# Kernel tuning notes

Hardware: AMD Instinct MI355X
Metric: run time of the kernel (lower is better)

## Reference

```python
import jax, jax.numpy as jnp
import numpy as np

T, B, N_IN, N_OUT = 100, 32, 1024, 512
LR_LTP, LR_LTD = 1e-4, -1e-4
TAU_PRE, TAU_POST, DT = 20.0, 20.0, 1.0
W_MIN, W_MAX = 0.0, 1.0
SPIKE_PROB = 0.05


def setup_inputs() -> dict:
    key = jax.random.key(0)
    k1, k2, k3 = jax.random.split(key, 3)
    weight = jax.random.uniform(k1, (N_OUT, N_IN), dtype=jnp.float32)
    pre_spikes = (jax.random.uniform(k2, (T, B, N_IN)) < SPIKE_PROB).astype(jnp.float32)
    post_spikes = (jax.random.uniform(k3, (T, B, N_OUT)) < SPIKE_PROB).astype(jnp.float32)
    pre_trace = jnp.zeros((B, N_IN), jnp.float32)
    post_trace = jnp.zeros((B, N_OUT), jnp.float32)
    return {"weight": weight, "pre_spikes": pre_spikes, "post_spikes": post_spikes,
            "pre_trace": pre_trace, "post_trace": post_trace}


def reference(weight, pre_spikes, post_spikes, pre_trace, post_trace):
    # weight: [N_out, N_in]; pre_spikes: [T,B,N_in]; post_spikes: [T,B,N_out]
    decay_pre = jnp.exp(jnp.asarray(-DT / TAU_PRE, weight.dtype))
    decay_post = jnp.exp(jnp.asarray(-DT / TAU_POST, weight.dtype))
    # Soft bounds (w_max=1.0 > 0 -> w_max - w; w_min=0.0 not < 0 -> w)
    soft_ltp = W_MAX - weight
    soft_ltd = weight
    Bf = jnp.asarray(pre_spikes.shape[1], weight.dtype)

    def step(carry, xs):
        pre_tr, post_tr, dw = carry
        pre_s, post_s = xs  # [B,N_in], [B,N_out]
        pre_tr = pre_tr * decay_pre + pre_s
        post_tr = post_tr * decay_post + post_s
        # batch-mean of outer products -> [N_out, N_in]
        ltp_mean = jnp.einsum('bo,bi->oi', post_s, pre_tr) / Bf
        ltd_mean = jnp.einsum('bo,bi->oi', post_tr, pre_s) / Bf
        dw = dw + LR_LTP * soft_ltp * ltp_mean + LR_LTD * soft_ltd * ltd_mean
        return (pre_tr, post_tr, dw), None

    init = (pre_trace, post_trace, jnp.zeros_like(weight))
    (pre_tr, post_tr, delta_w), _ = jax.lax.scan(step, init, (pre_spikes, post_spikes))
    return delta_w, pre_tr, post_tr
```

## Files before the change

### kernel.cpp

```cpp
#include <hip/hip_runtime.h>

typedef unsigned short ushort;
typedef __attribute__((ext_vector_type(8))) short short8;
typedef __attribute__((ext_vector_type(8))) ushort ushort8;
typedef __attribute__((ext_vector_type(4))) float floatx4;

#define T_STEPS 100
#define BATCH   32
#define NIN     1024
#define NOUT    512
#define KTOT    (T_STEPS * BATCH)
#define KBYTES  (KTOT * 2)

#define LR_LTP  (1e-4f)
#define LR_LTD  (-1e-4f)
#define INV_B   (1.0f / 32.0f)
#define DECAY   0.951229424500714f

#define OFF_PRE  (NOUT * NIN)
#define OFF_POST (OFF_PRE + BATCH * NIN)

#define U_WSPRE   0
#define U_WSPOST  (U_WSPRE + KTOT * NIN)
#define U_PRST    (U_WSPOST + KTOT * NOUT)
#define U_POST_ST (U_PRST + NIN * KTOT)
#define U_PRTT    (U_POST_ST + NOUT * KTOT)
#define U_POTT    (U_PRTT + NIN * KTOT)
#define U_END     (U_POTT + NOUT * KTOT)

static __device__ __forceinline__ ushort f2bf(float f) {
    union { float f; unsigned int u; } v; v.f = f;
    unsigned int r = (v.u + 0x7FFFu + ((v.u >> 16) & 1u)) >> 16;
    return (ushort)r;
}

__global__ __launch_bounds__(256) void stdp_traces(
    const float* __restrict__ pre_s,
    const float* __restrict__ post_s,
    const float* __restrict__ pre_tr0,
    const float* __restrict__ post_tr0,
    ushort* __restrict__ ws_pre16,
    ushort* __restrict__ ws_post16,
    float* __restrict__ out)
{
    const int tid = blockIdx.x * blockDim.x + threadIdx.x;
    if (tid < BATCH * NIN) {
        float tr = pre_tr0[tid];
        for (int t0 = 0; t0 < T_STEPS; t0 += 10) {
            float s[10];
            #pragma unroll
            for (int j = 0; j < 10; ++j)
                s[j] = pre_s[(size_t)(t0 + j) * (BATCH * NIN) + tid];
            #pragma unroll
            for (int j = 0; j < 10; ++j) {
                tr = tr * DECAY + s[j];
                ws_pre16[(size_t)(t0 + j) * (BATCH * NIN) + tid] = f2bf(tr);
            }
        }
        out[OFF_PRE + tid] = tr;
    } else {
        const int id = tid - BATCH * NIN;
        if (id < BATCH * NOUT) {
            float tr = post_tr0[id];
            for (int t0 = 0; t0 < T_STEPS; t0 += 10) {
                float s[10];
                #pragma unroll
                for (int j = 0; j < 10; ++j)
                    s[j] = post_s[(size_t)(t0 + j) * (BATCH * NOUT) + id];
                #pragma unroll
                for (int j = 0; j < 10; ++j) {
                    tr = tr * DECAY + s[j];
                    ws_post16[(size_t)(t0 + j) * (BATCH * NOUT) + id] = f2bf(tr);
                }
            }
            out[OFF_POST + id] = tr;
        }
    }
}

__global__ __launch_bounds__(256) void stdp_transpose(
    const float* __restrict__ pre_s, const float* __restrict__ post_s,
    const ushort* __restrict__ ws_pre16, const ushort* __restrict__ ws_post16,
    ushort* __restrict__ pre_s_t, ushort* __restrict__ post_s_t,
    ushort* __restrict__ pre_tr_t, ushort* __restrict__ post_tr_t)
{
    __shared__ ushort tile[64][72];

    const int y = blockIdx.y;
    const float* srcF = nullptr;
    const ushort* srcH = nullptr;
    ushort* dst; int ncols, n0;
    if (y < 16)       { srcF = pre_s;     dst = pre_s_t;  ncols = NIN;  n0 = y * 64; }
    else if (y < 24)  { srcF = post_s;    dst = post_s_t; ncols = NOUT; n0 = (y - 16) * 64; }
    else if (y < 40)  { srcH = ws_pre16;  dst = pre_tr_t; ncols = NIN;  n0 = (y - 24) * 64; }
    else              { srcH = ws_post16; dst = post_tr_t; ncols = NOUT; n0 = (y - 40) * 64; }

    const int k0 = blockIdx.x * 64;
    const int r  = threadIdx.x >> 2;
    const int cq = threadIdx.x & 3;

    if (srcF) {
        const float* s = srcF + (size_t)(k0 + r) * ncols + n0 + cq * 16;
        ushort tmp[16];
        #pragma unroll
        for (int v = 0; v < 4; ++v) {
            const float4 f = ((const float4*)s)[v];
            tmp[v * 4 + 0] = f2bf(f.x); tmp[v * 4 + 1] = f2bf(f.y);
            tmp[v * 4 + 2] = f2bf(f.z); tmp[v * 4 + 3] = f2bf(f.w);
        }
        *(ushort8*)&tile[r][cq * 16]     = *(const ushort8*)&tmp[0];
        *(ushort8*)&tile[r][cq * 16 + 8] = *(const ushort8*)&tmp[8];
    } else {
        const ushort* s = srcH + (size_t)(k0 + r) * ncols + n0 + cq * 16;
        *(ushort8*)&tile[r][cq * 16]     = ((const ushort8*)s)[0];
        *(ushort8*)&tile[r][cq * 16 + 8] = ((const ushort8*)s)[1];
    }
    __syncthreads();

    union { ushort u[16]; ushort8 v[2]; } o;
    #pragma unroll
    for (int j = 0; j < 16; ++j) o.u[j] = tile[cq * 16 + j][r];
    ushort* d = dst + (size_t)(n0 + r) * KTOT + k0 + cq * 16;
    ((ushort8*)d)[0] = o.v[0];
    ((ushort8*)d)[1] = o.v[1];
}

__global__ __launch_bounds__(256) void stdp_mfma_gemm(
    const ushort* __restrict__ post_s_t, const ushort* __restrict__ pre_tr_t,
    const ushort* __restrict__ post_tr_t, const ushort* __restrict__ pre_s_t,
    float* __restrict__ Spart, int kchunk)
{
    __shared__ ushort As[128 * 32];
    __shared__ ushort Bs[128 * 32];

    const int z = blockIdx.z;
    const ushort* Ag = (z & 1) ? post_tr_t : post_s_t;
    const ushort* Bg = (z & 1) ? pre_s_t   : pre_tr_t;
    const int i0 = blockIdx.x * 128;
    const int o0 = blockIdx.y * 128;
    const int k0 = (z >> 1) * kchunk;

    const int tid  = threadIdx.x;
    const int w    = tid >> 6;
    const int lane = tid & 63;
    const int quad = lane >> 4;
    const int l16  = lane & 15;
    const int wm   = w & 1;
    const int wn   = w >> 1;

    floatx4 acc[4][4];
    const floatx4 zero4 = {0.f, 0.f, 0.f, 0.f};
    #pragma unroll
    for (int mt = 0; mt < 4; ++mt)
        #pragma unroll
        for (int nt = 0; nt < 4; ++nt) acc[mt][nt] = zero4;

    for (int kb = k0; kb < k0 + kchunk; kb += 32) {
        #pragma unroll
        for (int q = 0; q < 2; ++q) {
            const int c   = w * 128 + q * 64 + lane;
            const int row = c >> 2;
            const int kob = (c & 3) * 16;
            const char* ga = (const char*)Ag + (size_t)(o0 + row) * KBYTES + kb * 2 + kob;
            const char* gb = (const char*)Bg + (size_t)(i0 + row) * KBYTES + kb * 2 + kob;
            __builtin_amdgcn_global_load_lds(
                (const __attribute__((address_space(1))) void*)ga,
                (__attribute__((address_space(3))) void*)((char*)As + w * 2048 + q * 1024),
                16, 0, 0);
            __builtin_amdgcn_global_load_lds(
                (const __attribute__((address_space(1))) void*)gb,
                (__attribute__((address_space(3))) void*)((char*)Bs + w * 2048 + q * 1024),
                16, 0, 0);
        }
        __syncthreads();

        short8 a[4], b[4];
        #pragma unroll
        for (int mt = 0; mt < 4; ++mt)
            a[mt] = *(const short8*)&As[(wm * 64 + mt * 16 + l16) * 32 + quad * 8];
        #pragma unroll
        for (int nt = 0; nt < 4; ++nt)
            b[nt] = *(const short8*)&Bs[(wn * 64 + nt * 16 + l16) * 32 + quad * 8];
        #pragma unroll
        for (int mt = 0; mt < 4; ++mt)
            #pragma unroll
            for (int nt = 0; nt < 4; ++nt)
                acc[mt][nt] = __builtin_amdgcn_mfma_f32_16x16x32_bf16(
                    a[mt], b[nt], acc[mt][nt], 0, 0, 0);
        __syncthreads();
    }

    float* S = Spart + (size_t)z * (NOUT * NIN);
    const int r0 = quad * 4;
    #pragma unroll
    for (int mt = 0; mt < 4; ++mt) {
        const int obase = o0 + wm * 64 + mt * 16 + r0;
        #pragma unroll
        for (int nt = 0; nt < 4; ++nt) {
            const int i = i0 + wn * 64 + nt * 16 + l16;
            #pragma unroll
            for (int r = 0; r < 4; ++r)
                S[(size_t)(obase + r) * NIN + i] = acc[mt][nt][r];
        }
    }
}

__global__ __launch_bounds__(256) void stdp_finalize(
    const float* __restrict__ w,
    const float* __restrict__ Spart,
    float* __restrict__ out, int nslab)
{
    const int j = blockIdx.x * blockDim.x + threadIdx.x;
    const float4 wv = ((const float4*)w)[j];
    float4 sp = make_float4(0.f, 0.f, 0.f, 0.f);
    float4 sd = make_float4(0.f, 0.f, 0.f, 0.f);
    for (int s = 0; s < nslab; s += 2) {
        const float4 p = ((const float4*)(Spart + (size_t)s       * (NOUT * NIN)))[j];
        const float4 d = ((const float4*)(Spart + (size_t)(s + 1) * (NOUT * NIN)))[j];
        sp.x += p.x; sp.y += p.y; sp.z += p.z; sp.w += p.w;
        sd.x += d.x; sd.y += d.y; sd.z += d.z; sd.w += d.w;
    }
    float4 o;
    o.x = LR_LTP * (1.0f - wv.x) * sp.x * INV_B + LR_LTD * wv.x * sd.x * INV_B;
    o.y = LR_LTP * (1.0f - wv.y) * sp.y * INV_B + LR_LTD * wv.y * sd.y * INV_B;
    o.z = LR_LTP * (1.0f - wv.z) * sp.z * INV_B + LR_LTD * wv.z * sd.z * INV_B;
    o.w = LR_LTP * (1.0f - wv.w) * sp.w * INV_B + LR_LTD * wv.w * sd.w * INV_B;
    ((float4*)out)[j] = o;
}

extern "C" void kernel_launch(void* const* d_in, const int* in_sizes, int n_in,
                              void* d_out, int out_size, void* d_ws, size_t ws_size,
                              hipStream_t stream) {
    const float* weight   = (const float*)d_in[0];
    const float* pre_s    = (const float*)d_in[1];
    const float* post_s   = (const float*)d_in[2];
    const float* pre_tr0  = (const float*)d_in[3];
    const float* post_tr0 = (const float*)d_in[4];
    float* out = (float*)d_out;

    ushort* u = (ushort*)d_ws;
    ushort* ws_pre16  = u + U_WSPRE;
    ushort* ws_post16 = u + U_WSPOST;
    ushort* pre_s_t   = u + U_PRST;
    ushort* post_s_t  = u + U_POST_ST;
    ushort* pre_tr_t  = u + U_PRTT;
    ushort* post_tr_t = u + U_POTT;
    float*  Spart     = (float*)((char*)d_ws + (size_t)U_END * 2);

    const size_t fixed_bytes = (size_t)U_END * 2;
    const size_t slab_bytes  = (size_t)NOUT * NIN * 4;
    int KS = 1;
    const int cand[5] = {10, 5, 4, 2, 1};
    for (int c = 0; c < 5; ++c) {
        if (fixed_bytes + (size_t)2 * cand[c] * slab_bytes <= ws_size) { KS = cand[c]; break; }
    }
    const int kchunk = KTOT / KS;

    stdp_traces<<<dim3((BATCH * NIN + BATCH * NOUT) / 256), dim3(256), 0, stream>>>(
        pre_s, post_s, pre_tr0, post_tr0, ws_pre16, ws_post16, out);

    stdp_transpose<<<dim3(KTOT / 64, 48), dim3(256), 0, stream>>>(
        pre_s, post_s, ws_pre16, ws_post16, pre_s_t, post_s_t, pre_tr_t, post_tr_t);

    stdp_mfma_gemm<<<dim3(NIN / 128, NOUT / 128, 2 * KS), dim3(256), 0, stream>>>(
        post_s_t, pre_tr_t, post_tr_t, pre_s_t, Spart, kchunk);

    stdp_finalize<<<dim3((NOUT * NIN / 4) / 256), dim3(256), 0, stream>>>(
        weight, Spart, out, 2 * KS);
}
```

Measured before the change: 115.4 us.

## Fuse trace scan with transpose and fold finalize into dual GEMM via atomics

The trace kernel now packs each thread's 100-step spike and trace history in registers as bf16, then writes it directly in transposed, K-padded layout (batch-major segments of 112). This removes the separate transpose kernel and the intermediate trace buffers. The GEMM computes the LTP and LTD products in one block with two accumulators and applies the soft-bound weight epilogue in place. It atomically adds split-K partials into an output zeroed by the first kernel, which removes the partial-sum slabs and the finalize kernel. The costs are heavy register use in the trace kernel, uncoalesced per-thread row writes, and atomic contention across 8 K splits.

```diff
diff --git a/kernel.cpp b/kernel.cpp
--- a/kernel.cpp
+++ b/kernel.cpp
@@ -2,15 +2,19 @@
 
 typedef unsigned short ushort;
 typedef __attribute__((ext_vector_type(8))) short short8;
-typedef __attribute__((ext_vector_type(8))) ushort ushort8;
 typedef __attribute__((ext_vector_type(4))) float floatx4;
 
 #define T_STEPS 100
 #define BATCH   32
 #define NIN     1024
 #define NOUT    512
-#define KTOT    (T_STEPS * BATCH)
-#define KBYTES  (KTOT * 2)
+
+#define SEG     112
+#define KPAD    (BATCH * SEG)
+#define KPADB   (KPAD * 2)
+#define KS      8
+#define KCHUNK  (KPAD / KS)
+#define BK      32
 
 #define LR_LTP  (1e-4f)
 #define LR_LTD  (-1e-4f)
@@ -20,13 +24,10 @@
 #define OFF_PRE  (NOUT * NIN)
 #define OFF_POST (OFF_PRE + BATCH * NIN)
 
-#define U_WSPRE   0
-#define U_WSPOST  (U_WSPRE + KTOT * NIN)
-#define U_PRST    (U_WSPOST + KTOT * NOUT)
-#define U_POST_ST (U_PRST + NIN * KTOT)
-#define U_PRTT    (U_POST_ST + NOUT * KTOT)
-#define U_POTT    (U_PRTT + NIN * KTOT)
-#define U_END     (U_POTT + NOUT * KTOT)
+#define U_PRST  0
+#define U_PRTT  (U_PRST + NIN * KPAD)
+#define U_POST  (U_PRTT + NIN * KPAD)
+#define U_POTT  (U_POST + NOUT * KPAD)
 
 static __device__ __forceinline__ ushort f2bf(float f) {
     union { float f; unsigned int u; } v; v.f = f;
@@ -34,111 +35,88 @@
     return (ushort)r;
 }
 
-__global__ __launch_bounds__(256) void stdp_traces(
+__global__ __launch_bounds__(256, 1) void stdp_traces_t(
     const float* __restrict__ pre_s,
     const float* __restrict__ post_s,
     const float* __restrict__ pre_tr0,
     const float* __restrict__ post_tr0,
-    ushort* __restrict__ ws_pre16,
-    ushort* __restrict__ ws_post16,
+    ushort* __restrict__ pre_s_t, ushort* __restrict__ pre_tr_t,
+    ushort* __restrict__ post_s_t, ushort* __restrict__ post_tr_t,
     float* __restrict__ out)
 {
     const int tid = blockIdx.x * blockDim.x + threadIdx.x;
+
+    {
+        const float4 z4 = make_float4(0.f, 0.f, 0.f, 0.f);
+        #pragma unroll
+        for (int k = 0; k < 3; ++k) {
+            const int j = tid + k * (BATCH * (NIN + NOUT));
+            if (j < (NOUT * NIN) / 4) ((float4*)out)[j] = z4;
+        }
+    }
+
+    unsigned int trp[56];
+    unsigned int spp[56];
+    #pragma unroll
+    for (int j = 50; j < 56; ++j) { trp[j] = 0u; spp[j] = 0u; }
+
+    const float* src; const float* init;
+    ushort *dst_s, *dst_t;
+    int nch, id, outoff;
     if (tid < BATCH * NIN) {
-        float tr = pre_tr0[tid];
-        for (int t0 = 0; t0 < T_STEPS; t0 += 10) {
-            float s[10];
-            #pragma unroll
-            for (int j = 0; j < 10; ++j)
-                s[j] = pre_s[(size_t)(t0 + j) * (BATCH * NIN) + tid];
-            #pragma unroll
-            for (int j = 0; j < 10; ++j) {
-                tr = tr * DECAY + s[j];
-                ws_pre16[(size_t)(t0 + j) * (BATCH * NIN) + tid] = f2bf(tr);
-            }
-        }
-        out[OFF_PRE + tid] = tr;
+        src = pre_s;  init = pre_tr0;  dst_s = pre_s_t;  dst_t = pre_tr_t;
+        nch = NIN;  id = tid;               outoff = OFF_PRE;
     } else {
-        const int id = tid - BATCH * NIN;
-        if (id < BATCH * NOUT) {
-            float tr = post_tr0[id];
-            for (int t0 = 0; t0 < T_STEPS; t0 += 10) {
-                float s[10];
-                #pragma unroll
-                for (int j = 0; j < 10; ++j)
-                    s[j] = post_s[(size_t)(t0 + j) * (BATCH * NOUT) + id];
-                #pragma unroll
-                for (int j = 0; j < 10; ++j) {
-                    tr = tr * DECAY + s[j];
-                    ws_post16[(size_t)(t0 + j) * (BATCH * NOUT) + id] = f2bf(tr);
-                }
-            }
-            out[OFF_POST + id] = tr;
-        }
-    }
-}
-
-__global__ __launch_bounds__(256) void stdp_transpose(
-    const float* __restrict__ pre_s, const float* __restrict__ post_s,
-    const ushort* __restrict__ ws_pre16, const ushort* __restrict__ ws_post16,
-    ushort* __restrict__ pre_s_t, ushort* __restrict__ post_s_t,
-    ushort* __restrict__ pre_tr_t, ushort* __restrict__ post_tr_t)
-{
-    __shared__ ushort tile[64][72];
-
-    const int y = blockIdx.y;
-    const float* srcF = nullptr;
-    const ushort* srcH = nullptr;
-    ushort* dst; int ncols, n0;
-    if (y < 16)       { srcF = pre_s;     dst = pre_s_t;  ncols = NIN;  n0 = y * 64; }
-    else if (y < 24)  { srcF = post_s;    dst = post_s_t; ncols = NOUT; n0 = (y - 16) * 64; }
-    else if (y < 40)  { srcH = ws_pre16;  dst = pre_tr_t; ncols = NIN;  n0 = (y - 24) * 64; }
-    else              { srcH = ws_post16; dst = post_tr_t; ncols = NOUT; n0 = (y - 40) * 64; }
-
-    const int k0 = blockIdx.x * 64;
-    const int r  = threadIdx.x >> 2;
-    const int cq = threadIdx.x & 3;
-
-    if (srcF) {
-        const float* s = srcF + (size_t)(k0 + r) * ncols + n0 + cq * 16;
-        ushort tmp[16];
-        #pragma unroll
-        for (int v = 0; v < 4; ++v) {
-            const float4 f = ((const float4*)s)[v];
-            tmp[v * 4 + 0] = f2bf(f.x); tmp[v * 4 + 1] = f2bf(f.y);
-            tmp[v * 4 + 2] = f2bf(f.z); tmp[v * 4 + 3] = f2bf(f.w);
-        }
-        *(ushort8*)&tile[r][cq * 16]     = *(const ushort8*)&tmp[0];
-        *(ushort8*)&tile[r][cq * 16 + 8] = *(const ushort8*)&tmp[8];
-    } else {
-        const ushort* s = srcH + (size_t)(k0 + r) * ncols + n0 + cq * 16;
-        *(ushort8*)&tile[r][cq * 16]     = ((const ushort8*)s)[0];
-        *(ushort8*)&tile[r][cq * 16 + 8] = ((const ushort8*)s)[1];
-    }
-    __syncthreads();
-
-    union { ushort u[16]; ushort8 v[2]; } o;
-    #pragma unroll
-    for (int j = 0; j < 16; ++j) o.u[j] = tile[cq * 16 + j][r];
-    ushort* d = dst + (size_t)(n0 + r) * KTOT + k0 + cq * 16;
-    ((ushort8*)d)[0] = o.v[0];
-    ((ushort8*)d)[1] = o.v[1];
-}
-
-__global__ __launch_bounds__(256) void stdp_mfma_gemm(
+        src = post_s; init = post_tr0; dst_s = post_s_t; dst_t = post_tr_t;
+        nch = NOUT; id = tid - BATCH * NIN; outoff = OFF_POST;
+    }
+
+    const size_t stride = (size_t)BATCH * nch;
+    float tr = init[id];
+    #pragma unroll
+    for (int t0 = 0; t0 < T_STEPS; t0 += 10) {
+        float s[10];
+        #pragma unroll
+        for (int j = 0; j < 10; ++j)
+            s[j] = src[(size_t)(t0 + j) * stride + id];
+        #pragma unroll
+        for (int j = 0; j < 10; ++j) {
+            const int t = t0 + j;
+            tr = tr * DECAY + s[j];
+            const unsigned int tb = (unsigned int)f2bf(tr);
+            const unsigned int sb = (unsigned int)f2bf(s[j]);
+            if (t & 1) { trp[t >> 1] |= tb << 16; spp[t >> 1] |= sb << 16; }
+            else       { trp[t >> 1]  = tb;       spp[t >> 1]  = sb;       }
+        }
+    }
+    out[outoff + id] = tr;
+
+    const int b  = id / nch;
+    const int ch = id - b * nch;
+    ushort* rs = dst_s + (size_t)ch * KPAD + b * SEG;
+    ushort* rt = dst_t + (size_t)ch * KPAD + b * SEG;
+    #pragma unroll
+    for (int c = 0; c < 14; ++c) {
+        const uint4 vs = make_uint4(spp[4*c], spp[4*c+1], spp[4*c+2], spp[4*c+3]);
+        const uint4 vt = make_uint4(trp[4*c], trp[4*c+1], trp[4*c+2], trp[4*c+3]);
+        ((uint4*)rs)[c] = vs;
+        ((uint4*)rt)[c] = vt;
+    }
+}
+
+__global__ __launch_bounds__(256) void stdp_gemm_dual(
     const ushort* __restrict__ post_s_t, const ushort* __restrict__ pre_tr_t,
     const ushort* __restrict__ post_tr_t, const ushort* __restrict__ pre_s_t,
-    float* __restrict__ Spart, int kchunk)
+    const float* __restrict__ wmat, float* __restrict__ out)
 {
-    __shared__ ushort As[128 * 32];
-    __shared__ ushort Bs[128 * 32];
-
-    const int z = blockIdx.z;
-    const ushort* Ag = (z & 1) ? post_tr_t : post_s_t;
-    const ushort* Bg = (z & 1) ? pre_s_t   : pre_tr_t;
+    __shared__ ushort AsP[128 * 32];
+    __shared__ ushort AsD[128 * 32];
+    __shared__ ushort BsP[128 * 32];
+    __shared__ ushort BsD[128 * 32];
+
     const int i0 = blockIdx.x * 128;
     const int o0 = blockIdx.y * 128;
-    const int k0 = (z >> 1) * kchunk;
+    const int k0 = blockIdx.z * KCHUNK;
 
     const int tid  = threadIdx.x;
     const int w    = tid >> 6;
@@ -148,84 +126,81 @@
     const int wm   = w & 1;
     const int wn   = w >> 1;
 
-    floatx4 acc[4][4];
+    floatx4 accP[4][4];
+    floatx4 accD[4][4];
     const floatx4 zero4 = {0.f, 0.f, 0.f, 0.f};
     #pragma unroll
     for (int mt = 0; mt < 4; ++mt)
         #pragma unroll
-        for (int nt = 0; nt < 4; ++nt) acc[mt][nt] = zero4;
-
-    for (int kb = k0; kb < k0 + kchunk; kb += 32) {
+        for (int nt = 0; nt < 4; ++nt) { accP[mt][nt] = zero4; accD[mt][nt] = zero4; }
+
+    for (int kb = k0; kb < k0 + KCHUNK; kb += BK) {
         #pragma unroll
         for (int q = 0; q < 2; ++q) {
             const int c   = w * 128 + q * 64 + lane;
             const int row = c >> 2;
             const int kob = (c & 3) * 16;
-            const char* ga = (const char*)Ag + (size_t)(o0 + row) * KBYTES + kb * 2 + kob;
-            const char* gb = (const char*)Bg + (size_t)(i0 + row) * KBYTES + kb * 2 + kob;
-            __builtin_amdgcn_global_load_lds(
-                (const __attribute__((address_space(1))) void*)ga,
-                (__attribute__((address_space(3))) void*)((char*)As + w * 2048 + q * 1024),
-                16, 0, 0);
-            __builtin_amdgcn_global_load_lds(
-                (const __attribute__((address_space(1))) void*)gb,
-                (__attribute__((address_space(3))) void*)((char*)Bs + w * 2048 + q * 1024),
-                16, 0, 0);
+            const size_t aoff = (size_t)(o0 + row) * KPADB + kb * 2 + kob;
+            const size_t boff = (size_t)(i0 + row) * KPADB + kb * 2 + kob;
+            const int ldso = w * 2048 + q * 1024;
+            __builtin_amdgcn_global_load_lds(
+                (const __attribute__((address_space(1))) void*)((const char*)post_s_t + aoff),
+                (__attribute__((address_space(3))) void*)((char*)AsP + ldso), 16, 0, 0);
+            __builtin_amdgcn_global_load_lds(
+                (const __attribute__((address_space(1))) void*)((const char*)post_tr_t + aoff),
+                (__attribute__((address_space(3))) void*)((char*)AsD + ldso), 16, 0, 0);
+            __builtin_amdgcn_global_load_lds(
+                (const __attribute__((address_space(1))) void*)((const char*)pre_tr_t + boff),
+                (__attribute__((address_space(3))) void*)((char*)BsP + ldso), 16, 0, 0);
+            __builtin_amdgcn_global_load_lds(
+                (const __attribute__((address_space(1))) void*)((const char*)pre_s_t + boff),
+                (__attribute__((address_space(3))) void*)((char*)BsD + ldso), 16, 0, 0);
         }
         __syncthreads();
 
-        short8 a[4], b[4];
-        #pragma unroll
-        for (int mt = 0; mt < 4; ++mt)
-            a[mt] = *(const short8*)&As[(wm * 64 + mt * 16 + l16) * 32 + quad * 8];
-        #pragma unroll
-        for (int nt = 0; nt < 4; ++nt)
-            b[nt] = *(const short8*)&Bs[(wn * 64 + nt * 16 + l16) * 32 + quad * 8];
+        short8 aP[4], aD[4], bP[4], bD[4];
+        #pragma unroll
+        for (int mt = 0; mt < 4; ++mt) {
+            const int r = (wm * 64 + mt * 16 + l16) * 32 + quad * 8;
+            aP[mt] = *(const short8*)&AsP[r];
+            aD[mt] = *(const short8*)&AsD[r];
+        }
+        #pragma unroll
+        for (int nt = 0; nt < 4; ++nt) {
+            const int r = (wn * 64 + nt * 16 + l16) * 32 + quad * 8;
+            bP[nt] = *(const short8*)&BsP[r];
+            bD[nt] = *(const short8*)&BsD[r];
+        }
         #pragma unroll
         for (int mt = 0; mt < 4; ++mt)
             #pragma unroll
-            for (int nt = 0; nt < 4; ++nt)
-                acc[mt][nt] = __builtin_amdgcn_mfma_f32_16x16x32_bf16(
-                    a[mt], b[nt], acc[mt][nt], 0, 0, 0);
+            for (int nt = 0; nt < 4; ++nt) {
+                accP[mt][nt] = __builtin_amdgcn_mfma_f32_16x16x32_bf16(
+                    aP[mt], bP[nt], accP[mt][nt], 0, 0, 0);
+                accD[mt][nt] = __builtin_amdgcn_mfma_f32_16x16x32_bf16(
+                    aD[mt], bD[nt], accD[mt][nt], 0, 0, 0);
+            }
         __syncthreads();
     }
 
-    float* S = Spart + (size_t)z * (NOUT * NIN);
-    const int r0 = quad * 4;
+    const float c1 = LR_LTP * INV_B;
+    const float c2 = LR_LTD * INV_B;
     #pragma unroll
     for (int mt = 0; mt < 4; ++mt) {
-        const int obase = o0 + wm * 64 + mt * 16 + r0;
+        const int obase = o0 + wm * 64 + mt * 16 + quad * 4;
         #pragma unroll
         for (int nt = 0; nt < 4; ++nt) {
             const int i = i0 + wn * 64 + nt * 16 + l16;
             #pragma unroll
-            for (int r = 0; r < 4; ++r)
-                S[(size_t)(obase + r) * NIN + i] = acc[mt][nt][r];
-        }
-    }
-}
-
-__global__ __launch_bounds__(256) void stdp_finalize(
-    const float* __restrict__ w,
-    const float* __restrict__ Spart,
-    float* __restrict__ out, int nslab)
-{
-    const int j = blockIdx.x * blockDim.x + threadIdx.x;
-    const float4 wv = ((const float4*)w)[j];
-    float4 sp = make_float4(0.f, 0.f, 0.f, 0.f);
-    float4 sd = make_float4(0.f, 0.f, 0.f, 0.f);
-    for (int s = 0; s < nslab; s += 2) {
-        const float4 p = ((const float4*)(Spart + (size_t)s       * (NOUT * NIN)))[j];
-        const float4 d = ((const float4*)(Spart + (size_t)(s + 1) * (NOUT * NIN)))[j];
-        sp.x += p.x; sp.y += p.y; sp.z += p.z; sp.w += p.w;
-        sd.x += d.x; sd.y += d.y; sd.z += d.z; sd.w += d.w;
-    }
-    float4 o;
-    o.x = LR_LTP * (1.0f - wv.x) * sp.x * INV_B + LR_LTD * wv.x * sd.x * INV_B;
-    o.y = LR_LTP * (1.0f - wv.y) * sp.y * INV_B + LR_LTD * wv.y * sd.y * INV_B;
-    o.z = LR_LTP * (1.0f - wv.z) * sp.z * INV_B + LR_LTD * wv.z * sd.z * INV_B;
-    o.w = LR_LTP * (1.0f - wv.w) * sp.w * INV_B + LR_LTD * wv.w * sd.w * INV_B;
-    ((float4*)out)[j] = o;
+            for (int r = 0; r < 4; ++r) {
+                const size_t idx = (size_t)(obase + r) * NIN + i;
+                const float wv = wmat[idx];
+                const float v = c1 * (1.0f - wv) * accP[mt][nt][r]
+                              + c2 * wv          * accD[mt][nt][r];
+                atomicAdd(&out[idx], v);
+            }
+        }
+    }
 }
 
 extern "C" void kernel_launch(void* const* d_in, const int* in_sizes, int n_in,
@@ -239,32 +214,15 @@
     float* out = (float*)d_out;
 
     ushort* u = (ushort*)d_ws;
-    ushort* ws_pre16  = u + U_WSPRE;
-    ushort* ws_post16 = u + U_WSPOST;
     ushort* pre_s_t   = u + U_PRST;
-    ushort* post_s_t  = u + U_POST_ST;
     ushort* pre_tr_t  = u + U_PRTT;
+    ushort* post_s_t  = u + U_POST;
     ushort* post_tr_t = u + U_POTT;
-    float*  Spart     = (float*)((char*)d_ws + (size_t)U_END * 2);
-
-    const size_t fixed_bytes = (size_t)U_END * 2;
-    const size_t slab_bytes  = (size_t)NOUT * NIN * 4;
-    int KS = 1;
-    const int cand[5] = {10, 5, 4, 2, 1};
-    for (int c = 0; c < 5; ++c) {
-        if (fixed_bytes + (size_t)2 * cand[c] * slab_bytes <= ws_size) { KS = cand[c]; break; }
-    }
-    const int kchunk = KTOT / KS;
-
-    stdp_traces<<<dim3((BATCH * NIN + BATCH * NOUT) / 256), dim3(256), 0, stream>>>(
-        pre_s, post_s, pre_tr0, post_tr0, ws_pre16, ws_post16, out);
-
-    stdp_transpose<<<dim3(KTOT / 64, 48), dim3(256), 0, stream>>>(
-        pre_s, post_s, ws_pre16, ws_post16, pre_s_t, post_s_t, pre_tr_t, post_tr_t);
-
-    stdp_mfma_gemm<<<dim3(NIN / 128, NOUT / 128, 2 * KS), dim3(256), 0, stream>>>(
-        post_s_t, pre_tr_t, post_tr_t, pre_s_t, Spart, kchunk);
-
-    stdp_finalize<<<dim3((NOUT * NIN / 4) / 256), dim3(256), 0, stream>>>(
-        weight, Spart, out, 2 * KS);
-}
+
+    stdp_traces_t<<<dim3(BATCH * (NIN + NOUT) / 256), dim3(256), 0, stream>>>(
+        pre_s, post_s, pre_tr0, post_tr0,
+        pre_s_t, pre_tr_t, post_s_t, post_tr_t, out);
+
+    stdp_gemm_dual<<<dim3(NIN / 128, NOUT / 128, KS), dim3(256), 0, stream>>>(
+        post_s_t, pre_tr_t, post_tr_t, pre_s_t, weight, out);
+}
```

Measured after the change: 127.6 us. 1.11x slower.

## Fuse dual GEMMs with epilogue atomics and chunk-parallel trace scan

Applied to the files above, without the earlier changes.

The trace kernel now splits the 100-step recurrence into four 25-step chunks per chain and combines them through shared-memory carry propagation. It also zeroes the output. The GEMM kernel computes both the LTP and LTD products in one 64x64 tile, applies the soft-bound weighting in its epilogue, and accumulates K-split partials into the output with atomicAdd. This removes the finalize kernel and the partial-slab writes and reads. In exchange it adds atomic contention across 5 K-splits, smaller tiles with less reuse, and order-dependent float summation.

```diff
diff --git a/kernel.cpp b/kernel.cpp
--- a/kernel.cpp
+++ b/kernel.cpp
@@ -10,12 +10,19 @@
 #define NIN     1024
 #define NOUT    512
 #define KTOT    (T_STEPS * BATCH)
-#define KBYTES  (KTOT * 2)
+#define KROWB   (KTOT * 2)
+
+#define KS      5
+#define KCHUNK  (KTOT / KS)
+#define BK      32
 
 #define LR_LTP  (1e-4f)
 #define LR_LTD  (-1e-4f)
 #define INV_B   (1.0f / 32.0f)
 #define DECAY   0.951229424500714f
+#define D25     0.286504796860190f
+#define TCH     25
+#define NCHUNK  4
 
 #define OFF_PRE  (NOUT * NIN)
 #define OFF_POST (OFF_PRE + BATCH * NIN)
@@ -26,7 +33,6 @@
 #define U_POST_ST (U_PRST + NIN * KTOT)
 #define U_PRTT    (U_POST_ST + NOUT * KTOT)
 #define U_POTT    (U_PRTT + NIN * KTOT)
-#define U_END     (U_POTT + NOUT * KTOT)
 
 static __device__ __forceinline__ ushort f2bf(float f) {
     union { float f; unsigned int u; } v; v.f = f;
@@ -43,39 +49,54 @@
     ushort* __restrict__ ws_post16,
     float* __restrict__ out)
 {
-    const int tid = blockIdx.x * blockDim.x + threadIdx.x;
-    if (tid < BATCH * NIN) {
-        float tr = pre_tr0[tid];
-        for (int t0 = 0; t0 < T_STEPS; t0 += 10) {
-            float s[10];
-            #pragma unroll
-            for (int j = 0; j < 10; ++j)
-                s[j] = pre_s[(size_t)(t0 + j) * (BATCH * NIN) + tid];
-            #pragma unroll
-            for (int j = 0; j < 10; ++j) {
-                tr = tr * DECAY + s[j];
-                ws_pre16[(size_t)(t0 + j) * (BATCH * NIN) + tid] = f2bf(tr);
-            }
-        }
-        out[OFF_PRE + tid] = tr;
+    __shared__ float Eend[NCHUNK][64];
+
+    {
+        const int j = blockIdx.x * 256 + threadIdx.x;
+        if (j < (NOUT * NIN) / 4)
+            ((float4*)out)[j] = make_float4(0.f, 0.f, 0.f, 0.f);
+    }
+
+    const int chain = threadIdx.x & 63;
+    const int c     = threadIdx.x >> 6;
+    int gchain = blockIdx.x * 64 + chain;
+
+    const float* src; const float* init; ushort* dst;
+    int id, stride, outoff;
+    if (gchain < BATCH * NIN) {
+        src = pre_s;  init = pre_tr0;  dst = ws_pre16;
+        id = gchain;  stride = BATCH * NIN;  outoff = OFF_PRE;
     } else {
-        const int id = tid - BATCH * NIN;
-        if (id < BATCH * NOUT) {
-            float tr = post_tr0[id];
-            for (int t0 = 0; t0 < T_STEPS; t0 += 10) {
-                float s[10];
-                #pragma unroll
-                for (int j = 0; j < 10; ++j)
-                    s[j] = post_s[(size_t)(t0 + j) * (BATCH * NOUT) + id];
-                #pragma unroll
-                for (int j = 0; j < 10; ++j) {
-                    tr = tr * DECAY + s[j];
-                    ws_post16[(size_t)(t0 + j) * (BATCH * NOUT) + id] = f2bf(tr);
-                }
-            }
-            out[OFF_POST + id] = tr;
-        }
-    }
+        src = post_s; init = post_tr0; dst = ws_post16;
+        id = gchain - BATCH * NIN; stride = BATCH * NOUT; outoff = OFF_POST;
+    }
+
+    const int t0 = c * TCH;
+    float x[TCH];
+    #pragma unroll
+    for (int m = 0; m < TCH; ++m)
+        x[m] = src[(size_t)(t0 + m) * stride + id];
+
+    float e = 0.f;
+    #pragma unroll
+    for (int m = 0; m < TCH; ++m) { e = e * DECAY + x[m]; x[m] = e; }
+    Eend[c][chain] = e;
+    __syncthreads();
+
+    float C = init[id];
+    for (int cc = 0; cc < c; ++cc)
+        C = C * D25 + Eend[cc][chain];
+
+    float p = C * DECAY;
+    #pragma unroll
+    for (int m = 0; m < TCH; ++m) { x[m] += p; p *= DECAY; }
+
+    #pragma unroll
+    for (int m = 0; m < TCH; ++m)
+        dst[(size_t)(t0 + m) * stride + id] = f2bf(x[m]);
+
+    if (c == NCHUNK - 1)
+        out[outoff + id] = x[TCH - 1];
 }
 
 __global__ __launch_bounds__(256) void stdp_transpose(
@@ -90,9 +111,9 @@
     const float* srcF = nullptr;
     const ushort* srcH = nullptr;
     ushort* dst; int ncols, n0;
-    if (y < 16)       { srcF = pre_s;     dst = pre_s_t;  ncols = NIN;  n0 = y * 64; }
-    else if (y < 24)  { srcF = post_s;    dst = post_s_t; ncols = NOUT; n0 = (y - 16) * 64; }
-    else if (y < 40)  { srcH = ws_pre16;  dst = pre_tr_t; ncols = NIN;  n0 = (y - 24) * 64; }
+    if (y < 16)       { srcF = pre_s;     dst = pre_s_t;   ncols = NIN;  n0 = y * 64; }
+    else if (y < 24)  { srcF = post_s;    dst = post_s_t;  ncols = NOUT; n0 = (y - 16) * 64; }
+    else if (y < 40)  { srcH = ws_pre16;  dst = pre_tr_t;  ncols = NIN;  n0 = (y - 24) * 64; }
     else              { srcH = ws_post16; dst = post_tr_t; ncols = NOUT; n0 = (y - 40) * 64; }
 
     const int k0 = blockIdx.x * 64;
@@ -125,20 +146,16 @@
     ((ushort8*)d)[1] = o.v[1];
 }
 
-__global__ __launch_bounds__(256) void stdp_mfma_gemm(
-    const ushort* __restrict__ post_s_t, const ushort* __restrict__ pre_tr_t,
-    const ushort* __restrict__ post_tr_t, const ushort* __restrict__ pre_s_t,
-    float* __restrict__ Spart, int kchunk)
+__global__ __launch_bounds__(256) void stdp_gemm_dual(
+    const ushort* __restrict__ post_s_t, const ushort* __restrict__ post_tr_t,
+    const ushort* __restrict__ pre_tr_t, const ushort* __restrict__ pre_s_t,
+    const float* __restrict__ wmat, float* __restrict__ out)
 {
-    __shared__ ushort As[128 * 32];
-    __shared__ ushort Bs[128 * 32];
-
-    const int z = blockIdx.z;
-    const ushort* Ag = (z & 1) ? post_tr_t : post_s_t;
-    const ushort* Bg = (z & 1) ? pre_s_t   : pre_tr_t;
-    const int i0 = blockIdx.x * 128;
-    const int o0 = blockIdx.y * 128;
-    const int k0 = (z >> 1) * kchunk;
+    __shared__ ushort S[4 * 2048];
+
+    const int i0 = blockIdx.x * 64;
+    const int o0 = blockIdx.y * 64;
+    const int k0 = blockIdx.z * KCHUNK;
 
     const int tid  = threadIdx.x;
     const int w    = tid >> 6;
@@ -148,84 +165,80 @@
     const int wm   = w & 1;
     const int wn   = w >> 1;
 
-    floatx4 acc[4][4];
+    const ushort* gbase;
+    {
+        const ushort* t;
+        if (w == 0)      t = post_s_t  + (size_t)o0 * KTOT;
+        else if (w == 1) t = post_tr_t + (size_t)o0 * KTOT;
+        else if (w == 2) t = pre_tr_t  + (size_t)i0 * KTOT;
+        else             t = pre_s_t   + (size_t)i0 * KTOT;
+        gbase = t;
+    }
+
+    floatx4 accP[2][2], accD[2][2];
     const floatx4 zero4 = {0.f, 0.f, 0.f, 0.f};
     #pragma unroll
-    for (int mt = 0; mt < 4; ++mt)
-        #pragma unroll
-        for (int nt = 0; nt < 4; ++nt) acc[mt][nt] = zero4;
-
-    for (int kb = k0; kb < k0 + kchunk; kb += 32) {
-        #pragma unroll
-        for (int q = 0; q < 2; ++q) {
-            const int c   = w * 128 + q * 64 + lane;
-            const int row = c >> 2;
-            const int kob = (c & 3) * 16;
-            const char* ga = (const char*)Ag + (size_t)(o0 + row) * KBYTES + kb * 2 + kob;
-            const char* gb = (const char*)Bg + (size_t)(i0 + row) * KBYTES + kb * 2 + kob;
+    for (int mt = 0; mt < 2; ++mt)
+        #pragma unroll
+        for (int nt = 0; nt < 2; ++nt) { accP[mt][nt] = zero4; accD[mt][nt] = zero4; }
+
+    for (int kb = k0; kb < k0 + KCHUNK; kb += BK) {
+        #pragma unroll
+        for (int q = 0; q < 4; ++q) {
+            const int chunk = q * 64 + lane;
+            const int row   = chunk >> 2;
+            const int kob   = (chunk & 3) * 16;
+            const char* g = (const char*)gbase + (size_t)row * KROWB + kb * 2 + kob;
             __builtin_amdgcn_global_load_lds(
-                (const __attribute__((address_space(1))) void*)ga,
-                (__attribute__((address_space(3))) void*)((char*)As + w * 2048 + q * 1024),
+                (const __attribute__((address_space(1))) void*)g,
+                (__attribute__((address_space(3))) void*)((char*)S + w * 4096 + q * 1024),
                 16, 0, 0);
-            __builtin_amdgcn_global_load_lds(
-                (const __attribute__((address_space(1))) void*)gb,
-                (__attribute__((address_space(3))) void*)((char*)Bs + w * 2048 + q * 1024),
-                16, 0, 0);
         }
         __syncthreads();
 
-        short8 a[4], b[4];
-        #pragma unroll
-        for (int mt = 0; mt < 4; ++mt)
-            a[mt] = *(const short8*)&As[(wm * 64 + mt * 16 + l16) * 32 + quad * 8];
-        #pragma unroll
-        for (int nt = 0; nt < 4; ++nt)
-            b[nt] = *(const short8*)&Bs[(wn * 64 + nt * 16 + l16) * 32 + quad * 8];
-        #pragma unroll
-        for (int mt = 0; mt < 4; ++mt)
+        short8 aP[2], aD[2], bP[2], bD[2];
+        #pragma unroll
+        for (int mt = 0; mt < 2; ++mt) {
+            const int r = (wm * 32 + mt * 16 + l16) * 32 + quad * 8;
+            aP[mt] = *(const short8*)&S[r];
+            aD[mt] = *(const short8*)&S[2048 + r];
+        }
+        #pragma unroll
+        for (int nt = 0; nt < 2; ++nt) {
+            const int r = (wn * 32 + nt * 16 + l16) * 32 + quad * 8;
+            bP[nt] = *(const short8*)&S[4096 + r];
+            bD[nt] = *(const short8*)&S[6144 + r];
+        }
+        #pragma unroll
+        for (int mt = 0; mt < 2; ++mt)
             #pragma unroll
-            for (int nt = 0; nt < 4; ++nt)
-                acc[mt][nt] = __builtin_amdgcn_mfma_f32_16x16x32_bf16(
-                    a[mt], b[nt], acc[mt][nt], 0, 0, 0);
+            for (int nt = 0; nt < 2; ++nt) {
+                accP[mt][nt] = __builtin_amdgcn_mfma_f32_16x16x32_bf16(
+                    aP[mt], bP[nt], accP[mt][nt], 0, 0, 0);
+                accD[mt][nt] = __builtin_amdgcn_mfma_f32_16x16x32_bf16(
+                    aD[mt], bD[nt], accD[mt][nt], 0, 0, 0);
+            }
         __syncthreads();
     }
 
-    float* S = Spart + (size_t)z * (NOUT * NIN);
-    const int r0 = quad * 4;
-    #pragma unroll
-    for (int mt = 0; mt < 4; ++mt) {
-        const int obase = o0 + wm * 64 + mt * 16 + r0;
-        #pragma unroll
-        for (int nt = 0; nt < 4; ++nt) {
-            const int i = i0 + wn * 64 + nt * 16 + l16;
+    const float c1 = LR_LTP * INV_B;
+    const float c2 = LR_LTD * INV_B;
+    #pragma unroll
+    for (int mt = 0; mt < 2; ++mt) {
+        const int obase = o0 + wm * 32 + mt * 16 + quad * 4;
+        #pragma unroll
+        for (int nt = 0; nt < 2; ++nt) {
+            const int i = i0 + wn * 32 + nt * 16 + l16;
             #pragma unroll
-            for (int r = 0; r < 4; ++r)
-                S[(size_t)(obase + r) * NIN + i] = acc[mt][nt][r];
-        }
-    }
-}
-
-__global__ __launch_bounds__(256) void stdp_finalize(
-    const float* __restrict__ w,
-    const float* __restrict__ Spart,
-    float* __restrict__ out, int nslab)
-{
-    const int j = blockIdx.x * blockDim.x + threadIdx.x;
-    const float4 wv = ((const float4*)w)[j];
-    float4 sp = make_float4(0.f, 0.f, 0.f, 0.f);
-    float4 sd = make_float4(0.f, 0.f, 0.f, 0.f);
-    for (int s = 0; s < nslab; s += 2) {
-        const float4 p = ((const float4*)(Spart + (size_t)s       * (NOUT * NIN)))[j];
-        const float4 d = ((const float4*)(Spart + (size_t)(s + 1) * (NOUT * NIN)))[j];
-        sp.x += p.x; sp.y += p.y; sp.z += p.z; sp.w += p.w;
-        sd.x += d.x; sd.y += d.y; sd.z += d.z; sd.w += d.w;
-    }
-    float4 o;
-    o.x = LR_LTP * (1.0f - wv.x) * sp.x * INV_B + LR_LTD * wv.x * sd.x * INV_B;
-    o.y = LR_LTP * (1.0f - wv.y) * sp.y * INV_B + LR_LTD * wv.y * sd.y * INV_B;
-    o.z = LR_LTP * (1.0f - wv.z) * sp.z * INV_B + LR_LTD * wv.z * sd.z * INV_B;
-    o.w = LR_LTP * (1.0f - wv.w) * sp.w * INV_B + LR_LTD * wv.w * sd.w * INV_B;
-    ((float4*)out)[j] = o;
+            for (int r = 0; r < 4; ++r) {
+                const size_t idx = (size_t)(obase + r) * NIN + i;
+                const float wv = wmat[idx];
+                const float v = c1 * (1.0f - wv) * accP[mt][nt][r]
+                              + c2 * wv          * accD[mt][nt][r];
+                atomicAdd(&out[idx], v);
+            }
+        }
+    }
 }
 
 extern "C" void kernel_launch(void* const* d_in, const int* in_sizes, int n_in,
@@ -245,26 +258,13 @@
     ushort* post_s_t  = u + U_POST_ST;
     ushort* pre_tr_t  = u + U_PRTT;
     ushort* post_tr_t = u + U_POTT;
-    float*  Spart     = (float*)((char*)d_ws + (size_t)U_END * 2);
-
-    const size_t fixed_bytes = (size_t)U_END * 2;
-    const size_t slab_bytes  = (size_t)NOUT * NIN * 4;
-    int KS = 1;
-    const int cand[5] = {10, 5, 4, 2, 1};
-    for (int c = 0; c < 5; ++c) {
-        if (fixed_bytes + (size_t)2 * cand[c] * slab_bytes <= ws_size) { KS = cand[c]; break; }
-    }
-    const int kchunk = KTOT / KS;
-
-    stdp_traces<<<dim3((BATCH * NIN + BATCH * NOUT) / 256), dim3(256), 0, stream>>>(
+
+    stdp_traces<<<dim3(BATCH * (NIN + NOUT) / 64), dim3(256), 0, stream>>>(
         pre_s, post_s, pre_tr0, post_tr0, ws_pre16, ws_post16, out);
 
     stdp_transpose<<<dim3(KTOT / 64, 48), dim3(256), 0, stream>>>(
         pre_s, post_s, ws_pre16, ws_post16, pre_s_t, post_s_t, pre_tr_t, post_tr_t);
 
-    stdp_mfma_gemm<<<dim3(NIN / 128, NOUT / 128, 2 * KS), dim3(256), 0, stream>>>(
-        post_s_t, pre_tr_t, post_tr_t, pre_s_t, Spart, kchunk);
-
-    stdp_finalize<<<dim3((NOUT * NIN / 4) / 256), dim3(256), 0, stream>>>(
-        weight, Spart, out, 2 * KS);
-}
+    stdp_gemm_dual<<<dim3(NIN / 64, NOUT / 64, KS), dim3(256), 0, stream>>>(
+        post_s_t, post_tr_t, pre_tr_t, pre_s_t, weight, out);
+}
```

Measured after the change: 111.8 us. 3.1% less time.
